# Kernel optimization log

Measured on AMD Instinct MI355X. Metric: run time of the kernel, lower is better.

Reference implementation:

```python
import jax, jax.numpy as jnp
import numpy as np

N, F, H, R, T, E, C = 50000, 128, 64, 3, 2, 500000, 2


def _seg_sum(v, idx, n):
    return jax.ops.segment_sum(v, idx, num_segments=n)


def _sage(x, src, dst, Wl, Wr, b, n):
    # PyG SAGEConv(mean): lin_l(mean_{j->i} x_j) + lin_r(x_i); lin_l carries bias.
    s = _seg_sum(x[src], dst, n)
    cnt = _seg_sum(jnp.ones((src.shape[0],), x.dtype), dst, n)
    agg = s / jnp.maximum(cnt, 1.0)[:, None]
    return agg @ Wl + x @ Wr + b


def _gcn(x, src, dst, w, W, b, n):
    # PyG GCNConv with edge_weight: self-loops (weight 1) + symmetric norm.
    deg = _seg_sum(w, dst, n) + 1.0
    dinv = deg ** -0.5
    norm = dinv[src] * w * dinv[dst]
    xW = x @ W
    return _seg_sum(norm[:, None] * xW[src], dst, n) + xW / deg[:, None] + b


def setup_inputs() -> dict:
    key = jax.random.key(0)
    ks = jax.random.split(key, 32)
    rn = lambda k, shp, s=0.1: jax.random.normal(k, shp, dtype=jnp.float32) * s
    return {
        "x": rn(ks[0], (N, F), 1.0),
        "edge_main": jax.random.randint(ks[1], (R, 2, E), 0, N, dtype=jnp.int32),
        "edge_tree": jax.random.randint(ks[2], (R, T, 2, E), 0, N, dtype=jnp.int32),
        "sage_Wl0": rn(ks[3], (R, F, H)), "sage_Wr0": rn(ks[4], (R, F, H)), "sage_b0": rn(ks[5], (R, H)),
        "sage_Wl1": rn(ks[6], (R, H, H)), "sage_Wr1": rn(ks[7], (R, H, H)), "sage_b1": rn(ks[8], (R, H)),
        "tree_Wl": rn(ks[9], (R, T, F, H)), "tree_Wr": rn(ks[10], (R, T, F, H)), "tree_b": rn(ks[11], (R, T, H)),
        "gate_W": rn(ks[12], (R, T, H)), "gate_b": rn(ks[13], (R, T)),
        "node_emb": rn(ks[14], (R, H), 1.0), "edge_emb": rn(ks[15], (R, H), 1.0),
        "fm_W": rn(ks[16], (R, 2 * H + F, F)), "fm_b": rn(ks[17], (R, F)),
        "ea_W1": rn(ks[18], (3 * H, F)), "ea_b1": rn(ks[19], (F,)),
        "ea_W2": rn(ks[20], (F, 1)), "ea_b2": rn(ks[21], (1,)),
        "gcn_W0": rn(ks[22], (R, F, H)), "gcn_b0": rn(ks[23], (R, H)),
        "gcn_W1": rn(ks[24], (R, H, H)), "gcn_b1": rn(ks[25], (R, H)),
        "lin_W": rn(ks[26], (R * H, C)), "lin_b": rn(ks[27], (C,)),
    }


def reference(x, edge_main, edge_tree, sage_Wl0, sage_Wr0, sage_b0, sage_Wl1, sage_Wr1, sage_b1,
              tree_Wl, tree_Wr, tree_b, gate_W, gate_b, node_emb, edge_emb, fm_W, fm_b,
              ea_W1, ea_b1, ea_W2, ea_b2, gcn_W0, gcn_b0, gcn_W1, gcn_b1, lin_W, lin_b):
    outs = []
    for r in range(R):
        src, dst = edge_main[r, 0], edge_main[r, 1]
        # Layer_AGG main SAGE stack (2 layers, relu between; dropout = eval no-op)
        y = jax.nn.relu(_sage(x, src, dst, sage_Wl0[r], sage_Wr0[r], sage_b0[r], N))
        y = _sage(y, src, dst, sage_Wl1[r], sage_Wr1[r], sage_b1[r], N)
        # tree branches + softmax gating
        trees = []
        for t in range(T):
            ts, td = edge_tree[r, t, 0], edge_tree[r, t, 1]
            trees.append(jax.nn.relu(_sage(x, ts, td, tree_Wl[r, t], tree_Wr[r, t], tree_b[r, t], N)))
        gates = jnp.stack([trees[t] @ gate_W[r, t] + gate_b[r, t] for t in range(T)], axis=-1)  # [N,T]
        alpha = jax.nn.softmax(gates, axis=-1)
        x_tree = sum(trees[t] * alpha[:, t:t + 1] for t in range(T))
        lo = y + 1.0 * x_tree  # self.weight = 1
        # edge mask via edge_attr_mlp on [lo[src], lo[dst], edge_type_emb]
        ef = jnp.concatenate([lo[src], lo[dst], jnp.broadcast_to(edge_emb[r], (E, H))], axis=-1)
        em = jax.nn.relu(ef @ ea_W1 + ea_b1) @ ea_W2 + ea_b2  # [E,1]
        # feature mask via feat_mask_r on [lo, x, node_type_emb]
        hetro = jnp.concatenate([lo, x, jnp.broadcast_to(node_emb[r], (N, H))], axis=-1)
        fm = hetro @ fm_W[r] + fm_b[r]
        mx = x * fm
        w = ((em - em.min()) / (em.max() - em.min()))[:, 0]  # min-max norm -> [E]
        # hetero GCN stack with edge weights
        z = jax.nn.relu(_gcn(mx, src, dst, w, gcn_W0[r], gcn_b0[r], N))
        z = _gcn(z, src, dst, w, gcn_W1[r], gcn_b1[r], N)
        outs.append(z)
    x_temp = jnp.concatenate(outs, axis=1)  # [N, R*H]
    logits = jnp.clip(x_temp @ lin_W + lin_b, -1e10, 1e10)
    return jax.nn.log_softmax(logits, axis=1), x_temp
```

## Files before the change

### kernel.cpp

```cpp
#include <hip/hip_runtime.h>
#include <cstdint>

#define N_NODES 50000
#define FEAT    128
#define HID     64
#define NREL    3
#define NTREE   2
#define NEDGE   500000
#define NCLS    2

#define BKT   391
#define CAP   1600
#define CHUNK 4096

typedef __attribute__((ext_vector_type(8))) short bfrag;
typedef __attribute__((ext_vector_type(4))) float ffrag;

__device__ __forceinline__ float wave_red(float v){
  #pragma unroll
  for(int off = 32; off > 0; off >>= 1) v += __shfl_xor(v, off, 64);
  return v;
}

__device__ __forceinline__ unsigned short f2b(float f){
// ... 102 lines not shown
    __syncthreads();
    if(tid < 128) sc[tid] += t;
    __syncthreads();
  }
  if(tid < 128){
    int excl = sc[tid] - h[tid];
    cur[tid] = excl;
    int node = b * 128 + tid;
    if(node < N_NODES) indptr9[(size_t)set * (N_NODES + 1) + node] = ebase + excl;
  }
  __syncthreads();
  for(int i = tid; i < cnt; i += 256){
    int p = pk[i];
    int r = atomicAdd(&cur[(p >> 16) & 127], 1);
    stage[r] = p & 0xFFFF;
  }
  __syncthreads();
  int* out = csr9 + (size_t)set * NEDGE + ebase;
  for(int i = tid; i < cnt; i += 256) out[i] = stage[i];
}

__global__ void k_tobf16(const float* __restrict__ in, unsigned short* __restrict__ o, int n4){
  int i = blockIdx.x * 256 + threadIdx.x;
  if(i < n4){
    float4 v = ((const float4*)in)[i];
    ushort4 u; u.x = f2b(v.x); u.y = f2b(v.y); u.z = f2b(v.z); u.w = f2b(v.w);
    ((ushort4*)o)[i] = u;
  }
}

struct PackJobs { const float* src[20]; int wst[20]; int K[20]; int dst[20]; int n; };

__global__ void k_wpack(PackJobs J, unsigned short* __restrict__ out){
  int j = blockIdx.x;
  if(j >= J.n) return;
  const float* s = J.src[j];
  int wst = J.wst[j], K = J.K[j];
  unsigned short* o = out + J.dst[j];
  for(int i = threadIdx.x; i < K * 64; i += 256){
    int k = i >> 6, c = i & 63;
    o[((((k >> 3) * 64) + c) << 3) + (k & 7)] = f2b(s[(size_t)k * wst + c]);
  }
}

struct MG {
  const unsigned short* Wt[4];
  const float* bias[4];
  const void* add[4];
  const float* mul[4];
  void* out[4];
  int ast, mst, ost;
};

template<int K1, int K2, int NGRP, int RELU, int HAS_ADD, int ADDB, int HAS_MUL, int OUT_BF16>
__global__ __launch_bounds__(256)
void k_mgemm(const unsigned short* __restrict__ X1, int xs1,
             const unsigned short* __restrict__ X2, int xs2, MG P){
  constexpr int K = K1 + K2;
  constexpr int KS = K / 32;
  int tid = threadIdx.x;
  int lane = tid & 63;
  int w = tid >> 6;
  int row0 = blockIdx.x * 64 + w * 16;
  int l15 = lane & 15, kg = lane >> 4;
  int arow = row0 + l15; if(arow > N_NODES - 1) arow = N_NODES - 1;
  bfrag a[KS];
  #pragma unroll
  for(int ks = 0; ks < KS; ks++){
    int kk = ks * 32 + kg * 8;
    const unsigned short* p = (kk < K1) ? (X1 + (size_t)arow * xs1 + kk)
                                        : (X2 + (size_t)arow * xs2 + (kk - K1));
    a[ks] = *(const bfrag*)p;
  }
  int orow0 = row0 + kg * 4;
  #pragma unroll
  for(int g = 0; g < NGRP; g++){
    const unsigned short* Wg = P.Wt[g];
    #pragma unroll
    for(int ct = 0; ct < 4; ct++){
      int col = ct * 16 + l15;
      ffrag acc = {0.f, 0.f, 0.f, 0.f};
      #pragma unroll
      for(int ks = 0; ks < KS; ks++){
        bfrag bf = *(const bfrag*)(Wg + (((size_t)(ks * 4 + kg) * 64 + col) << 3));
        acc = __builtin_amdgcn_mfma_f32_16x16x32_bf16(a[ks], bf, acc, 0, 0, 0);
      }
      float bv = P.bias[g] ? P.bias[g][col] : 0.f;
      #pragma unroll
      for(int i = 0; i < 4; i++){
        int r = orow0 + i;
        if(r >= N_NODES) break;
        float v = acc[i] + bv;
        if(HAS_ADD){
          if(ADDB) v += b2f(((const unsigned short*)P.add[g])[(size_t)r * P.ast + col]);
          else     v += ((const float*)P.add[g])[(size_t)r * P.ast + col];
        }
        if(RELU) v = fmaxf(v, 0.f);
        if(HAS_MUL) v *= P.mul[g][(size_t)r * P.mst + col];
        if(OUT_BF16) ((unsigned short*)P.out[g])[(size_t)r * P.ost + col] = f2b(v);
        else         ((float*)P.out[g])[(size_t)r * P.ost + col] = v;
      }
    }
  }
}

struct ABMX {
  const unsigned short* Wea[4];
  const unsigned short* Wfm[2];
  const float* cF;
  const float* xf32;
  unsigned short* ab;
  unsigned short* mx;
};

__global__ __launch_bounds__(256)
void k_abmx(const unsigned short* __restrict__ LOb, const unsigned short* __restrict__ xb, ABMX P){
  int tid = threadIdx.x, lane = tid & 63, w = tid >> 6;
  int row0 = blockIdx.x * 64 + w * 16;
  int l15 = lane & 15, kg = lane >> 4;
  int arow = row0 + l15; if(arow > N_NODES - 1) arow = N_NODES - 1;
  bfrag a[6];
  a[0] = *(const bfrag*)(LOb + (size_t)arow * 64 + kg * 8);
  a[1] = *(const bfrag*)(LOb + (size_t)arow * 64 + 32 + kg * 8);
  #pragma unroll
  for(int ks = 0; ks < 4; ks++)
    a[2 + ks] = *(const bfrag*)(xb + (size_t)arow * 128 + ks * 32 + kg * 8);
  int orow0 = row0 + kg * 4;
  #pragma unroll
  for(int g = 0; g < 4; g++){
    const unsigned short* Wg = P.Wea[g];
    #pragma unroll
    for(int ct = 0; ct < 4; ct++){
      int col = ct * 16 + l15;
      ffrag acc = {0.f, 0.f, 0.f, 0.f};
      bfrag b0 = *(const bfrag*)(Wg + (((size_t)(0 * 4 + kg) * 64 + col) << 3));
      bfrag b1 = *(const bfrag*)(Wg + (((size_t)(1 * 4 + kg) * 64 + col) << 3));
      acc = __builtin_amdgcn_mfma_f32_16x16x32_bf16(a[0], b0, acc, 0, 0, 0);
      acc = __builtin_amdgcn_mfma_f32_16x16x32_bf16(a[1], b1, acc, 0, 0, 0);
      #pragma unroll
      for(int i = 0; i < 4; i++){
        int r = orow0 + i;
        if(r >= N_NODES) break;
        P.ab[(size_t)r * 256 + g * 64 + col] = f2b(acc[i]);
      }
    }
  }
  #pragma unroll
  for(int g = 0; g < 2; g++){
    const unsigned short* Wg = P.Wfm[g];
    #pragma unroll
    for(int ct = 0; ct < 4; ct++){
      int col = ct * 16 + l15;
      ffrag acc = {0.f, 0.f, 0.f, 0.f};
      #pragma unroll
      for(int ks = 0; ks < 6; ks++){
        bfrag bf = *(const bfrag*)(Wg + (((size_t)(ks * 4 + kg) * 64 + col) << 3));
        acc = __builtin_amdgcn_mfma_f32_16x16x32_bf16(a[ks], bf, acc, 0, 0, 0);
      }
      float bv = P.cF[g * 64 + col];
      #pragma unroll
      for(int i = 0; i < 4; i++){
        int r = orow0 + i;
        if(r >= N_NODES) break;
        float v = (acc[i] + bv) * P.xf32[(size_t)r * 128 + g * 64 + col];
        P.mx[(size_t)r * 128 + g * 64 + col] = f2b(v);
      }
    }
  }
}

template<int OUTB>
__global__ void k_agg8(const unsigned short* __restrict__ TB, int tst,
                       const int* __restrict__ indptr, const int* __restrict__ csr,
                       void* __restrict__ out){
  int br = blockIdx.y;
  const unsigned short* T = TB + (size_t)br * tst;
  const int* ip = indptr + (size_t)br * (N_NODES + 1);
  const int* cs = csr + (size_t)br * NEDGE;
  int lane = threadIdx.x & 63, wid = threadIdx.x >> 6;
  int node = blockIdx.x * 4 + wid;
  if(node >= N_NODES) return;
  int q = lane >> 3, c = lane & 7;
  int beg = ip[node], end = ip[node + 1];
  int cnt = end - beg;
  float sc = 1.0f / (float)(cnt >= 1 ? cnt : 1);
  float a0=0.f,a1=0.f,a2=0.f,a3=0.f,a4=0.f,a5=0.f,a6=0.f,a7=0.f;
  int j = beg + q;
  for(; j + 8 < end; j += 16){
    int s0 = cs[j], s1 = cs[j + 8];
    uint4 u0 = *(const uint4*)(T + (size_t)s0 * 64 + c * 8);
    uint4 u1 = *(const uint4*)(T + (size_t)s1 * 64 + c * 8);
    a0 += b2f_lo(u0.x) + b2f_lo(u1.x); a1 += b2f_hi(u0.x) + b2f_hi(u1.x);
    a2 += b2f_lo(u0.y) + b2f_lo(u1.y); a3 += b2f_hi(u0.y) + b2f_hi(u1.y);
    a4 += b2f_lo(u0.z) + b2f_lo(u1.z); a5 += b2f_hi(u0.z) + b2f_hi(u1.z);
    a6 += b2f_lo(u0.w) + b2f_lo(u1.w); a7 += b2f_hi(u0.w) + b2f_hi(u1.w);
  }
  if(j < end){
    int s = cs[j];
    uint4 u = *(const uint4*)(T + (size_t)s * 64 + c * 8);
    a0 += b2f_lo(u.x); a1 += b2f_hi(u.x);
    a2 += b2f_lo(u.y); a3 += b2f_hi(u.y);
    a4 += b2f_lo(u.z); a5 += b2f_hi(u.z);
    a6 += b2f_lo(u.w); a7 += b2f_hi(u.w);
  }
  #pragma unroll
  for(int off = 8; off < 64; off <<= 1){
    a0 += __shfl_xor(a0, off, 64); a1 += __shfl_xor(a1, off, 64);
    a2 += __shfl_xor(a2, off, 64); a3 += __shfl_xor(a3, off, 64);
    a4 += __shfl_xor(a4, off, 64); a5 += __shfl_xor(a5, off, 64);
    a6 += __shfl_xor(a6, off, 64); a7 += __shfl_xor(a7, off, 64);
  }
  if(q == 0){
    if(OUTB){
      uint4 o;
      o.x = pk2(a0 * sc, a1 * sc); o.y = pk2(a2 * sc, a3 * sc);
      o.z = pk2(a4 * sc, a5 * sc); o.w = pk2(a6 * sc, a7 * sc);
      *(uint4*)((unsigned short*)out + (size_t)br * tst + (size_t)node * 64 + c * 8) = o;
    } else {
      float* o = (float*)out + (size_t)node * 64 + c * 8;
      *(float4*)o       = float4{a0 * sc, a1 * sc, a2 * sc, a3 * sc};
      *(float4*)(o + 4) = float4{a4 * sc, a5 * sc, a6 * sc, a7 * sc};
    }
  }
}

__global__ void k_gates_cvec(const unsigned short* __restrict__ t0b, const unsigned short* __restrict__ t1b,
                             const float* __restrict__ y, const float* __restrict__ gate_W,
                             const float* __restrict__ gate_b, unsigned short* __restrict__ lo,
                             const float* __restrict__ ee, const float* __restrict__ ne,
                             const float* __restrict__ eaW1, const float* __restrict__ eab1,
                             const float* __restrict__ fmW, const float* __restrict__ fmb,
                             float* __restrict__ cE, float* __restrict__ cF, int gn4){
  if(blockIdx.x >= gn4){
    int which = blockIdx.x - gn4;
    int j = threadIdx.x;
    if(j < 128){
      if(which == 0){
        float s = eab1[j];
        for(int k = 0; k < 64; k++) s += ee[k] * eaW1[(128 + k) * 128 + j];
        cE[j] = s;
      } else {
        float s = fmb[j];
        for(int k = 0; k < 64; k++) s += ne[k] * fmW[(192 + k) * 128 + j];
        cF[j] = s;
      }
    }
    return;
  }
  int lane = threadIdx.x & 63, wid = threadIdx.x >> 6;
  int node = blockIdx.x * 4 + wid;
  if(node >= N_NODES) return;
  size_t idx = (size_t)node * 64 + lane;
  float t0v = b2f(t0b[idx]), t1v = b2f(t1b[idx]), yv = y[idx];
  float g0 = wave_red(t0v * gate_W[lane]) + gate_b[0];
  float g1 = wave_red(t1v * gate_W[64 + lane]) + gate_b[1];
  float m = fmaxf(g0, g1);
  float e0 = expf(g0 - m), e1 = expf(g1 - m);
  float a0 = e0 / (e0 + e1);
  lo[idx] = f2b(yv + a0 * t0v + (1.f - a0) * t1v);
}

__global__ void k_em2(const unsigned short* __restrict__ AB,
                      const int* __restrict__ indptr, const int* __restrict__ csr_src,
                      const float* __restrict__ cvec, const float* __restrict__ W2,
                      const float* __restrict__ b2, float* __restrict__ em,
                      float* __restrict__ sumem, float* __restrict__ pmn, float* __restrict__ pmx){
  int lane = threadIdx.x & 63, wid = threadIdx.x >> 6;
  int node = blockIdx.x * 4 + wid;
  float mn = 3.4e38f, mx = -3.4e38f;
  if(node < N_NODES){
    int q = lane >> 4, c = lane & 15;
    uint4 bu = *(const uint4*)(AB + (size_t)node * 256 + 128 + c * 8);
    float4 cva = *(const float4*)&cvec[c * 8];
    float4 cvb = *(const float4*)&cvec[c * 8 + 4];
    float4 wva = *(const float4*)&W2[c * 8];
    float4 wvb = *(const float4*)&W2[c * 8 + 4];
    float cc0 = b2f_lo(bu.x) + cva.x, cc1 = b2f_hi(bu.x) + cva.y;
    float cc2 = b2f_lo(bu.y) + cva.z, cc3 = b2f_hi(bu.y) + cva.w;
    float cc4 = b2f_lo(bu.z) + cvb.x, cc5 = b2f_hi(bu.z) + cvb.y;
    float cc6 = b2f_lo(bu.w) + cvb.z, cc7 = b2f_hi(bu.w) + cvb.w;
    float b2v = b2[0];
    int beg = indptr[node], end = indptr[node + 1];
    float ssum = 0.f;
    int j = beg + q;
    for(; j + 4 < end; j += 8){
      int s0 = csr_src[j], s1 = csr_src[j + 4];
      uint4 u0 = *(const uint4*)(AB + (size_t)s0 * 256 + c * 8);
      uint4 u1 = *(const uint4*)(AB + (size_t)s1 * 256 + c * 8);
      float v0 = fmaxf(b2f_lo(u0.x) + cc0, 0.f) * wva.x + fmaxf(b2f_hi(u0.x) + cc1, 0.f) * wva.y
               + fmaxf(b2f_lo(u0.y) + cc2, 0.f) * wva.z + fmaxf(b2f_hi(u0.y) + cc3, 0.f) * wva.w
               + fmaxf(b2f_lo(u0.z) + cc4, 0.f) * wvb.x + fmaxf(b2f_hi(u0.z) + cc5, 0.f) * wvb.y
               + fmaxf(b2f_lo(u0.w) + cc6, 0.f) * wvb.z + fmaxf(b2f_hi(u0.w) + cc7, 0.f) * wvb.w;
      float v1 = fmaxf(b2f_lo(u1.x) + cc0, 0.f) * wva.x + fmaxf(b2f_hi(u1.x) + cc1, 0.f) * wva.y
               + fmaxf(b2f_lo(u1.y) + cc2, 0.f) * wva.z + fmaxf(b2f_hi(u1.y) + cc3, 0.f) * wva.w
               + fmaxf(b2f_lo(u1.z) + cc4, 0.f) * wvb.x + fmaxf(b2f_hi(u1.z) + cc5, 0.f) * wvb.y
               + fmaxf(b2f_lo(u1.w) + cc6, 0.f) * wvb.z + fmaxf(b2f_hi(u1.w) + cc7, 0.f) * wvb.w;
      #pragma unroll
      for(int off = 1; off < 16; off <<= 1){
        v0 += __shfl_xor(v0, off, 64);
        v1 += __shfl_xor(v1, off, 64);
      }
      float r0 = v0 + b2v, r1 = v1 + b2v;
      if(c == 0){ em[j] = r0; em[j + 4] = r1; }
      ssum += r0 + r1;
      mn = fminf(mn, fminf(r0, r1)); mx = fmaxf(mx, fmaxf(r0, r1));
    }
    if(j < end){
      int s = csr_src[j];
      uint4 u = *(const uint4*)(AB + (size_t)s * 256 + c * 8);
      float v = fmaxf(b2f_lo(u.x) + cc0, 0.f) * wva.x + fmaxf(b2f_hi(u.x) + cc1, 0.f) * wva.y
              + fmaxf(b2f_lo(u.y) + cc2, 0.f) * wva.z + fmaxf(b2f_hi(u.y) + cc3, 0.f) * wva.w
              + fmaxf(b2f_lo(u.z) + cc4, 0.f) * wvb.x + fmaxf(b2f_hi(u.z) + cc5, 0.f) * wvb.y
              + fmaxf(b2f_lo(u.w) + cc6, 0.f) * wvb.z + fmaxf(b2f_hi(u.w) + cc7, 0.f) * wvb.w;
      #pragma unroll
      for(int off = 1; off < 16; off <<= 1) v += __shfl_xor(v, off, 64);
      float r = v + b2v;
      if(c == 0) em[j] = r;
      ssum += r;
      mn = fminf(mn, r); mx = fmaxf(mx, r);
    }
    ssum += __shfl_xor(ssum, 16, 64); ssum += __shfl_xor(ssum, 32, 64);
    mn = fminf(mn, __shfl_xor(mn, 16, 64)); mn = fminf(mn, __shfl_xor(mn, 32, 64));
    mx = fmaxf(mx, __shfl_xor(mx, 16, 64)); mx = fmaxf(mx, __shfl_xor(mx, 32, 64));
    if(lane == 0) sumem[node] = ssum;
  }
  __shared__ float bmn[4], bmx[4];
  if(lane == 0){ bmn[wid] = mn; bmx[wid] = mx; }
  __syncthreads();
  if(threadIdx.x == 0){
    pmn[blockIdx.x] = fminf(fminf(bmn[0], bmn[1]), fminf(bmn[2], bmn[3]));
    pmx[blockIdx.x] = fmaxf(fmaxf(bmx[0], bmx[1]), fmaxf(bmx[2], bmx[3]));
  }
}

__global__ void k_minmax_final(const float* __restrict__ pmn, const float* __restrict__ pmx,
                               int nb, float* __restrict__ scal){
  __shared__ float smn[256], smx[256];
  int tid = threadIdx.x;
  float mn = 3.4e38f, mx = -3.4e38f;
  for(int i = tid; i < nb; i += 256){
    mn = fminf(mn, pmn[i]); mx = fmaxf(mx, pmx[i]);
  }
  smn[tid] = mn; smx[tid] = mx; __syncthreads();
  for(int s = 128; s > 0; s >>= 1){
    if(tid < s){ smn[tid] = fminf(smn[tid], smn[tid + s]); smx[tid] = fmaxf(smx[tid], smx[tid + s]); }
    __syncthreads();
  }
  if(tid == 0){
    scal[0] = smn[0];
    scal[1] = 1.0f / fmaxf(smx[0] - smn[0], 1e-30f);
  }
}

__global__ void k_dinv(const int* __restrict__ indptr, const float* __restrict__ sumem,
                       const float* __restrict__ scal, float* __restrict__ dinv){
  int i = blockIdx.x * 256 + threadIdx.x;
  if(i >= N_NODES) return;
  float mn = scal[0], inv = scal[1];
  float cnt = (float)(indptr[i + 1] - indptr[i]);
  dinv[i] = rsqrtf(1.f + (sumem[i] - cnt * mn) * inv);
}

template<int RELU, int OUTB>
__global__ void k_gcn(const unsigned short* __restrict__ xW, const int* __restrict__ indptr,
                      const int* __restrict__ csr_src, const float* __restrict__ em,
                      const float* __restrict__ scal, const float* __restrict__ dinv,
                      const float* __restrict__ bias, void* __restrict__ out, int ostride){
  int lane = threadIdx.x & 63, wid = threadIdx.x >> 6;
  int node = blockIdx.x * 4 + wid;
  if(node >= N_NODES) return;
  int q = lane >> 3, c = lane & 7;
  float mn = scal[0], inv = scal[1];
  float di = dinv[node];
  float a0=0.f,a1=0.f,a2=0.f,a3=0.f,a4=0.f,a5=0.f,a6=0.f,a7=0.f;
  int beg = indptr[node], end = indptr[node + 1];
  int j = beg + q;
  for(; j + 8 < end; j += 16){
    int s0 = csr_src[j], s1 = csr_src[j + 8];
    float w0 = (em[j] - mn) * inv * dinv[s0];
    float w1 = (em[j + 8] - mn) * inv * dinv[s1];
    uint4 u0 = *(const uint4*)(xW + (size_t)s0 * 64 + c * 8);
    uint4 u1 = *(const uint4*)(xW + (size_t)s1 * 64 + c * 8);
    a0 += w0 * b2f_lo(u0.x) + w1 * b2f_lo(u1.x); a1 += w0 * b2f_hi(u0.x) + w1 * b2f_hi(u1.x);
    a2 += w0 * b2f_lo(u0.y) + w1 * b2f_lo(u1.y); a3 += w0 * b2f_hi(u0.y) + w1 * b2f_hi(u1.y);
    a4 += w0 * b2f_lo(u0.z) + w1 * b2f_lo(u1.z); a5 += w0 * b2f_hi(u0.z) + w1 * b2f_hi(u1.z);
    a6 += w0 * b2f_lo(u0.w) + w1 * b2f_lo(u1.w); a7 += w0 * b2f_hi(u0.w) + w1 * b2f_hi(u1.w);
  }
  if(j < end){
    int s = csr_src[j];
    float wv = (em[j] - mn) * inv * dinv[s];
    uint4 u = *(const uint4*)(xW + (size_t)s * 64 + c * 8);
    a0 += wv * b2f_lo(u.x); a1 += wv * b2f_hi(u.x);
    a2 += wv * b2f_lo(u.y); a3 += wv * b2f_hi(u.y);
    a4 += wv * b2f_lo(u.z); a5 += wv * b2f_hi(u.z);
    a6 += wv * b2f_lo(u.w); a7 += wv * b2f_hi(u.w);
  }
  #pragma unroll
  for(int off = 8; off < 64; off <<= 1){
    a0 += __shfl_xor(a0, off, 64); a1 += __shfl_xor(a1, off, 64);
    a2 += __shfl_xor(a2, off, 64); a3 += __shfl_xor(a3, off, 64);
    a4 += __shfl_xor(a4, off, 64); a5 += __shfl_xor(a5, off, 64);
    a6 += __shfl_xor(a6, off, 64); a7 += __shfl_xor(a7, off, 64);
  }
  if(q == 0){
    uint4 su = *(const uint4*)(xW + (size_t)node * 64 + c * 8);
    float4 bva = *(const float4*)&bias[c * 8];
    float4 bvb = *(const float4*)&bias[c * 8 + 4];
    float dd = di * di;
    float r0 = a0 * di + b2f_lo(su.x) * dd + bva.x;
    float r1 = a1 * di + b2f_hi(su.x) * dd + bva.y;
    float r2 = a2 * di + b2f_lo(su.y) * dd + bva.z;
    float r3 = a3 * di + b2f_hi(su.y) * dd + bva.w;
    float r4 = a4 * di + b2f_lo(su.z) * dd + bvb.x;
// ... 33 lines not shown
  a1 = wave_red(a1);
  if(lane == 0){
    float l0 = fminf(fmaxf(a0 + lin_b[0], -1e10f), 1e10f);
    float l1 = fminf(fmaxf(a1 + lin_b[1], -1e10f), 1e10f);
    float m = fmaxf(l0, l1);
    float d = expf(l0 - m) + expf(l1 - m);
    float ls = m + logf(d);
    out[(size_t)node * 2 + 0] = l0 - ls;
    out[(size_t)node * 2 + 1] = l1 - ls;
  }
}

extern "C" void kernel_launch(void* const* d_in, const int* in_sizes, int n_in,
                              void* d_out, int out_size, void* d_ws, size_t ws_size,
                              hipStream_t stream){
  (void)in_sizes; (void)n_in; (void)out_size;
  const int N = N_NODES, E = NEDGE;

  const float* x        = (const float*)d_in[0];
  const int*  edge_main = (const int*)d_in[1];
  const int*  edge_tree = (const int*)d_in[2];
  const float* sage_Wl0 = (const float*)d_in[3];
  const float* sage_Wr0 = (const float*)d_in[4];
  const float* sage_b0  = (const float*)d_in[5];
  const float* sage_Wl1 = (const float*)d_in[6];
  const float* sage_Wr1 = (const float*)d_in[7];
  const float* sage_b1  = (const float*)d_in[8];
  const float* tree_Wl  = (const float*)d_in[9];
  const float* tree_Wr  = (const float*)d_in[10];
  const float* tree_b   = (const float*)d_in[11];
  const float* gate_W   = (const float*)d_in[12];
  const float* gate_b   = (const float*)d_in[13];
  const float* node_emb = (const float*)d_in[14];
  const float* edge_emb = (const float*)d_in[15];
  const float* fm_W     = (const float*)d_in[16];
  const float* fm_b     = (const float*)d_in[17];
  const float* ea_W1    = (const float*)d_in[18];
  const float* ea_b1    = (const float*)d_in[19];
  const float* ea_W2    = (const float*)d_in[20];
  const float* ea_b2    = (const float*)d_in[21];
  const float* gcn_W0   = (const float*)d_in[22];
  const float* gcn_b0   = (const float*)d_in[23];
  const float* gcn_W1   = (const float*)d_in[24];
  const float* gcn_b1   = (const float*)d_in[25];
  const float* lin_W    = (const float*)d_in[26];
  const float* lin_b    = (const float*)d_in[27];

  float* out_lsm   = (float*)d_out;
  float* out_xtemp = (float*)d_out + (size_t)N * NCLS;

  char* ws = (char*)d_ws;
  unsigned short* TB3  = (unsigned short*)(ws + 0);
  unsigned short* TBs  = (unsigned short*)(ws + 0);
  float*          Y    = (float*)(ws + 0);
  unsigned short* xW0b = (unsigned short*)(ws + 0);
  unsigned short* z0b  = (unsigned short*)(ws + 6400000);
  unsigned short* xW1b = (unsigned short*)(ws + 12800000);
  unsigned short* AG3  = (unsigned short*)(ws + 19200000);
  float*          AG   = (float*)(ws + 19200000);
  unsigned short* LOb  = (unsigned short*)(ws + 25600000);
  unsigned short* AB   = (unsigned short*)(ws + 0);
  unsigned short* y0b  = (unsigned short*)(ws + 38400000);
  unsigned short* T0b  = (unsigned short*)(ws + 44800000);
  unsigned short* T1b  = (unsigned short*)(ws + 51200000);
  unsigned short* MXb  = (unsigned short*)(ws + 38400000);
  unsigned short* xb   = (unsigned short*)(ws + 57600000);
  int*   bucketed = (int*)(ws + 0);
  unsigned short* Wpk = (unsigned short*)(ws + 70400000);
  int*   csr9     = (int*)(ws + 71000064);
  int*   indptr9  = (int*)(ws + 89000064);
  float* em       = (float*)(ws + 90800128);
  float* sumem    = (float*)(ws + 92800128);
  float* dinv     = (float*)(ws + 93000128);
  int*   cursor   = (int*)(ws + 93200128);
  int*   bktbase  = (int*)(ws + 93214208);
  float* cvecE    = (float*)(ws + 93228288);
  float* cvecF    = (float*)(ws + 93228800);
  float* scal     = (float*)(ws + 93229312);
  float* pmn      = (float*)(ws + 93229568);
  float* pmx      = (float*)(ws + 93279568);
  if(ws_size < 93330000) return;

  const int GN4 = (N + 3) / 4;
  const int GN  = (N + 255) / 256;
  const int GGM = (N + 63) / 64;
  const int NCH = (E + CHUNK - 1) / CHUNK;

  PackJobs PJ[2]; PJ[0].n = 0; PJ[1].n = 0;
  int npj = 0, dstElem = 0;
  const unsigned short* WlpA[NREL]; const unsigned short* WlpB[NREL]; const unsigned short* WlpC[NREL];
  const unsigned short* Wr0j[NREL]; const unsigned short* WrT0[NREL]; const unsigned short* WrT1[NREL];
  const unsigned short* Wl1j[NREL]; const unsigned short* Wr1j[NREL];
  const unsigned short* Fm0j[NREL]; const unsigned short* Fm1j[NREL];
  const unsigned short* G0j[NREL];  const unsigned short* G1j[NREL];
  const unsigned short *EaA0, *EaA1, *EaB0, *EaB1;
  auto addjob = [&](const float* src, int wst, int K) -> const unsigned short* {
    int slot = npj < 20 ? 0 : 1;
    int k = npj - slot * 20;
    PJ[slot].src[k] = src; PJ[slot].wst[k] = wst; PJ[slot].K[k] = K; PJ[slot].dst[k] = dstElem;
    PJ[slot].n = k + 1;
    const unsigned short* ret = Wpk + dstElem;
    dstElem += K * 64; npj++;
    return ret;
  };
  for(int r = 0; r < NREL; r++){
    WlpA[r] = addjob(sage_Wl0 + (size_t)r * 8192, 64, 128);
    WlpB[r] = addjob(tree_Wl + (size_t)(r * NTREE + 0) * 8192, 64, 128);
    WlpC[r] = addjob(tree_Wl + (size_t)(r * NTREE + 1) * 8192, 64, 128);
    Wr0j[r] = addjob(sage_Wr0 + (size_t)r * 8192, 64, 128);
    WrT0[r] = addjob(tree_Wr + (size_t)(r * NTREE + 0) * 8192, 64, 128);
    WrT1[r] = addjob(tree_Wr + (size_t)(r * NTREE + 1) * 8192, 64, 128);
    Wl1j[r] = addjob(sage_Wl1 + (size_t)r * 4096, 64, 64);
    Wr1j[r] = addjob(sage_Wr1 + (size_t)r * 4096, 64, 64);
    Fm0j[r] = addjob(fm_W + (size_t)r * 32768, 128, 192);
    Fm1j[r] = addjob(fm_W + (size_t)r * 32768 + 64, 128, 192);
    G0j[r]  = addjob(gcn_W0 + (size_t)r * 8192, 64, 128);
    G1j[r]  = addjob(gcn_W1 + (size_t)r * 4096, 64, 64);
  }
  EaA0 = addjob(ea_W1, 128, 64);
  EaA1 = addjob(ea_W1 + 64, 128, 64);
  EaB0 = addjob(ea_W1 + 64 * 128, 128, 64);
  EaB1 = addjob(ea_W1 + 64 * 128 + 64, 128, 64);

  EdgePtrs ep;
  for(int r = 0; r < NREL; r++){
    ep.s[r * 3 + 0] = edge_main + (size_t)r * 2 * E;
    ep.d[r * 3 + 0] = ep.s[r * 3 + 0] + E;
    for(int t = 0; t < NTREE; t++){
      ep.s[r * 3 + 1 + t] = edge_tree + ((size_t)(r * NTREE + t) * 2) * E;
      ep.d[r * 3 + 1 + t] = ep.s[r * 3 + 1 + t] + E;
    }
  }
  hipMemsetAsync(cursor, 0, 9 * BKT * 4, stream);
  k_passA<<<dim3(NCH, 9), 256, 0, stream>>>(ep, cursor, bucketed);
  k_scanB<<<9, 512, 0, stream>>>(cursor, bktbase, indptr9);
  k_passB<<<dim3(BKT, 9), 256, 0, stream>>>(bucketed, cursor, bktbase, indptr9, csr9);

  k_wpack<<<PJ[0].n, 256, 0, stream>>>(PJ[0], Wpk);
  k_wpack<<<PJ[1].n, 256, 0, stream>>>(PJ[1], Wpk);
  k_tobf16<<<(N * 128 / 4 + 255) / 256, 256, 0, stream>>>(x, xb, N * 128 / 4);

  for(int r = 0; r < NREL; r++){
    const int* ipM = indptr9 + (size_t)(r * 3) * (N + 1);
    const int* csM = csr9 + (size_t)(r * 3) * E;

    { MG p{}; p.ost = 64;
      p.Wt[0] = WlpA[r]; p.Wt[1] = WlpB[r]; p.Wt[2] = WlpC[r];
      p.out[0] = TB3; p.out[1] = TB3 + (size_t)N * 64; p.out[2] = TB3 + (size_t)2 * N * 64;
      k_mgemm<128, 0, 3, 0, 0, 0, 0, 1><<<GGM, 256, 0, stream>>>(xb, 128, nullptr, 0, p); }

    k_agg8<1><<<dim3(GN4, 3), 256, 0, stream>>>(TB3, N * 64, ipM, csM, AG3);
    { MG p{}; p.ast = 64; p.ost = 64;
      p.Wt[0] = Wr0j[r]; p.bias[0] = sage_b0 + r * 64; p.add[0] = AG3;                         p.out[0] = y0b;
      p.Wt[1] = WrT0[r]; p.bias[1] = tree_b + (size_t)(r * NTREE + 0) * 64; p.add[1] = AG3 + (size_t)N * 64;   p.out[1] = T0b;
      p.Wt[2] = WrT1[r]; p.bias[2] = tree_b + (size_t)(r * NTREE + 1) * 64; p.add[2] = AG3 + (size_t)2 * N * 64; p.out[2] = T1b;
      k_mgemm<128, 0, 3, 1, 1, 1, 0, 1><<<GGM, 256, 0, stream>>>(xb, 128, nullptr, 0, p); }

    { MG p{}; p.ost = 64; p.Wt[0] = Wl1j[r]; p.out[0] = TBs;
      k_mgemm<64, 0, 1, 0, 0, 0, 0, 1><<<GGM, 256, 0, stream>>>(y0b, 64, nullptr, 0, p); }
    k_agg8<0><<<dim3(GN4, 1), 256, 0, stream>>>(TBs, N * 64, ipM, csM, AG);
    { MG p{}; p.ast = 64; p.ost = 64;
      p.Wt[0] = Wr1j[r]; p.bias[0] = sage_b1 + r * 64; p.add[0] = AG; p.out[0] = Y;
      k_mgemm<64, 0, 1, 0, 1, 0, 0, 0><<<GGM, 256, 0, stream>>>(y0b, 64, nullptr, 0, p); }

    k_gates_cvec<<<GN4 + 2, 256, 0, stream>>>(T0b, T1b, Y, gate_W + (size_t)r * 128,
                                              gate_b + r * 2, LOb,
                                              edge_emb + r * 64, node_emb + r * 64,
                                              ea_W1, ea_b1, fm_W + (size_t)r * 32768,
                                              fm_b + r * 128, cvecE, cvecF, GN4);

    { ABMX p{};
      p.Wea[0] = EaA0; p.Wea[1] = EaA1; p.Wea[2] = EaB0; p.Wea[3] = EaB1;
      p.Wfm[0] = Fm0j[r]; p.Wfm[1] = Fm1j[r];
      p.cF = cvecF; p.xf32 = x; p.ab = AB; p.mx = MXb;
      k_abmx<<<GGM, 256, 0, stream>>>(LOb, xb, p); }

    k_em2<<<GN4, 256, 0, stream>>>(AB, ipM, csM, cvecE, ea_W2, ea_b2, em, sumem, pmn, pmx);

    k_minmax_final<<<1, 256, 0, stream>>>(pmn, pmx, GN4, scal);

    k_dinv<<<GN, 256, 0, stream>>>(ipM, sumem, scal, dinv);

    { MG p{}; p.ost = 64; p.Wt[0] = G0j[r]; p.out[0] = xW0b;
      k_mgemm<128, 0, 1, 0, 0, 0, 0, 1><<<GGM, 256, 0, stream>>>(MXb, 128, nullptr, 0, p); }
    k_gcn<1, 1><<<GN4, 256, 0, stream>>>(xW0b, ipM, csM, em, scal, dinv, gcn_b0 + r * 64, z0b, 64);
    { MG p{}; p.ost = 64; p.Wt[0] = G1j[r]; p.out[0] = xW1b;
      k_mgemm<64, 0, 1, 0, 0, 0, 0, 1><<<GGM, 256, 0, stream>>>(z0b, 64, nullptr, 0, p); }
    k_gcn<0, 0><<<GN4, 256, 0, stream>>>(xW1b, ipM, csM, em, scal, dinv, gcn_b1 + r * 64,
                                         out_xtemp + r * 64, 192);
  }

  k_logits<<<GN4, 256, 0, stream>>>(out_xtemp, lin_W, lin_b, out_lsm);
}
```

Baseline: 892.5 us.

## Fuse SAGE/tree GEMMs, gating and GCN xW0 into chained kernels per relation

Merges the post-aggregation SAGE/tree GEMM with the next layer's Wl1 projection through an LDS tile, fuses the Wr1 GEMM with tree gating and the lo computation, and chains the feature-mask product into the GCN layer-0 GEMM via shared memory. The min/max finalisation is folded into the dinv kernel, with each block redoing the small reduction. The aggregation kernel now uses 16 lanes of 4 columns per edge instead of 8 lanes of 8. The goal is fewer launches and fewer global round trips for intermediates such as Y, MX and the separate xW0 pass. The cost is extra LDS use and redundant reductions, and the workspace buffer aliasing is reshuffled.

```diff
diff --git a/kernel.cpp b/kernel.cpp
--- a/kernel.cpp
+++ b/kernel.cpp
@@ -178,12 +178,10 @@
   int ast, mst, ost;
 };
 
-template<int K1, int K2, int NGRP, int RELU, int HAS_ADD, int ADDB, int HAS_MUL, int OUT_BF16>
+template<int K1, int NGRP, int OUT_BF16>
 __global__ __launch_bounds__(256)
-void k_mgemm(const unsigned short* __restrict__ X1, int xs1,
-             const unsigned short* __restrict__ X2, int xs2, MG P){
-  constexpr int K = K1 + K2;
-  constexpr int KS = K / 32;
+void k_mgemm(const unsigned short* __restrict__ X1, int xs1, MG P){
+  constexpr int KS = K1 / 32;
   int tid = threadIdx.x;
   int lane = tid & 63;
   int w = tid >> 6;
@@ -192,12 +190,8 @@
   int arow = row0 + l15; if(arow > N_NODES - 1) arow = N_NODES - 1;
   bfrag a[KS];
   #pragma unroll
-  for(int ks = 0; ks < KS; ks++){
-    int kk = ks * 32 + kg * 8;
-    const unsigned short* p = (kk < K1) ? (X1 + (size_t)arow * xs1 + kk)
-                                        : (X2 + (size_t)arow * xs2 + (kk - K1));
-    a[ks] = *(const bfrag*)p;
-  }
+  for(int ks = 0; ks < KS; ks++)
+    a[ks] = *(const bfrag*)(X1 + (size_t)arow * xs1 + ks * 32 + kg * 8);
   int orow0 = row0 + kg * 4;
   #pragma unroll
   for(int g = 0; g < NGRP; g++){
@@ -211,18 +205,11 @@
         bfrag bf = *(const bfrag*)(Wg + (((size_t)(ks * 4 + kg) * 64 + col) << 3));
         acc = __builtin_amdgcn_mfma_f32_16x16x32_bf16(a[ks], bf, acc, 0, 0, 0);
       }
-      float bv = P.bias[g] ? P.bias[g][col] : 0.f;
       #pragma unroll
       for(int i = 0; i < 4; i++){
         int r = orow0 + i;
         if(r >= N_NODES) break;
-        float v = acc[i] + bv;
-        if(HAS_ADD){
-          if(ADDB) v += b2f(((const unsigned short*)P.add[g])[(size_t)r * P.ast + col]);
-          else     v += ((const float*)P.add[g])[(size_t)r * P.ast + col];
-        }
-        if(RELU) v = fmaxf(v, 0.f);
-        if(HAS_MUL) v *= P.mul[g][(size_t)r * P.mst + col];
+        float v = acc[i];
         if(OUT_BF16) ((unsigned short*)P.out[g])[(size_t)r * P.ost + col] = f2b(v);
         else         ((float*)P.out[g])[(size_t)r * P.ost + col] = v;
       }
@@ -230,17 +217,182 @@
   }
 }
 
-struct ABMX {
+struct S23 {
+  const unsigned short* Wr[3];
+  const float* bias[3];
+  const unsigned short* ag3;
+  const unsigned short* Wl1;
+  unsigned short *y0, *t0, *t1, *tbs;
+};
+
+__global__ __launch_bounds__(256)
+void k_s23(const unsigned short* __restrict__ xb, S23 P){
+  __shared__ unsigned short ytile[64][72];
+  int tid = threadIdx.x, lane = tid & 63, w = tid >> 6;
+  int row0 = blockIdx.x * 64 + w * 16;
+  int l15 = lane & 15, kg = lane >> 4;
+  int arow = row0 + l15; if(arow > N_NODES - 1) arow = N_NODES - 1;
+  bfrag a[4];
+  #pragma unroll
+  for(int ks = 0; ks < 4; ks++)
+    a[ks] = *(const bfrag*)(xb + (size_t)arow * 128 + ks * 32 + kg * 8);
+  int orow0 = row0 + kg * 4;
+  #pragma unroll
+  for(int g = 0; g < 3; g++){
+    const unsigned short* Wg = P.Wr[g];
+    unsigned short* og = (g == 0) ? P.y0 : (g == 1) ? P.t0 : P.t1;
+    #pragma unroll
+    for(int ct = 0; ct < 4; ct++){
+      int col = ct * 16 + l15;
+      ffrag acc = {0.f, 0.f, 0.f, 0.f};
+      #pragma unroll
+      for(int ks = 0; ks < 4; ks++){
+        bfrag bf = *(const bfrag*)(Wg + (((size_t)(ks * 4 + kg) * 64 + col) << 3));
+        acc = __builtin_amdgcn_mfma_f32_16x16x32_bf16(a[ks], bf, acc, 0, 0, 0);
+      }
+      float bv = P.bias[g][col];
+      #pragma unroll
+      for(int i = 0; i < 4; i++){
+        int r = orow0 + i;
+        int rr = (r < N_NODES) ? r : N_NODES - 1;
+        float v = acc[i] + bv + b2f(P.ag3[(size_t)g * N_NODES * 64 + (size_t)rr * 64 + col]);
+        v = fmaxf(v, 0.f);
+        unsigned short hh = f2b(v);
+        if(g == 0) ytile[w * 16 + kg * 4 + i][col] = hh;
+        if(r < N_NODES) og[(size_t)r * 64 + col] = hh;
+      }
+    }
+  }
+  __syncthreads();
+  bfrag a2[2];
+  a2[0] = *(const bfrag*)&ytile[w * 16 + l15][kg * 8];
+  a2[1] = *(const bfrag*)&ytile[w * 16 + l15][32 + kg * 8];
+  #pragma unroll
+  for(int ct = 0; ct < 4; ct++){
+    int col = ct * 16 + l15;
+    ffrag acc = {0.f, 0.f, 0.f, 0.f};
+    bfrag b0 = *(const bfrag*)(P.Wl1 + (((size_t)(0 * 4 + kg) * 64 + col) << 3));
+    bfrag b1 = *(const bfrag*)(P.Wl1 + (((size_t)(1 * 4 + kg) * 64 + col) << 3));
+    acc = __builtin_amdgcn_mfma_f32_16x16x32_bf16(a2[0], b0, acc, 0, 0, 0);
+    acc = __builtin_amdgcn_mfma_f32_16x16x32_bf16(a2[1], b1, acc, 0, 0, 0);
+    #pragma unroll
+    for(int i = 0; i < 4; i++){
+      int r = orow0 + i;
+      if(r >= N_NODES) break;
+      P.tbs[(size_t)r * 64 + col] = f2b(acc[i]);
+    }
+  }
+}
+
+struct YG {
+  const unsigned short* Wr1;
+  const float* b1;
+  const float* AG;
+  const unsigned short *t0b, *t1b;
+  const float *gate_W, *gate_b;
+  unsigned short* lo;
+  const float *ee, *ne, *eaW1, *eab1, *fmW, *fmb;
+  float *cE, *cF;
+  int ggm;
+};
+
+__global__ __launch_bounds__(256)
+void k_ygates(const unsigned short* __restrict__ y0b, YG P){
+  if(blockIdx.x >= P.ggm){
+    int which = blockIdx.x - P.ggm;
+    int j = threadIdx.x;
+    if(j < 128){
+      if(which == 0){
+        float s = P.eab1[j];
+        for(int k = 0; k < 64; k++) s += P.ee[k] * P.eaW1[(128 + k) * 128 + j];
+        P.cE[j] = s;
+      } else {
+        float s = P.fmb[j];
+        for(int k = 0; k < 64; k++) s += P.ne[k] * P.fmW[(192 + k) * 128 + j];
+        P.cF[j] = s;
+      }
+    }
+    return;
+  }
+  int tid = threadIdx.x, lane = tid & 63, w = tid >> 6;
+  int row0 = blockIdx.x * 64 + w * 16;
+  int l15 = lane & 15, kg = lane >> 4;
+  int arow = row0 + l15; if(arow > N_NODES - 1) arow = N_NODES - 1;
+  bfrag a0f = *(const bfrag*)(y0b + (size_t)arow * 64 + kg * 8);
+  bfrag a1f = *(const bfrag*)(y0b + (size_t)arow * 64 + 32 + kg * 8);
+  int orow0 = row0 + kg * 4;
+  float vv[4][4], t0v[4][4], t1v[4][4];
+  float gw0[4], gw1[4];
+  #pragma unroll
+  for(int ct = 0; ct < 4; ct++){
+    int col = ct * 16 + l15;
+    gw0[ct] = P.gate_W[col];
+    gw1[ct] = P.gate_W[64 + col];
+  }
+  #pragma unroll
+  for(int ct = 0; ct < 4; ct++){
+    int col = ct * 16 + l15;
+    ffrag acc = {0.f, 0.f, 0.f, 0.f};
+    bfrag b0 = *(const bfrag*)(P.Wr1 + (((size_t)(0 * 4 + kg) * 64 + col) << 3));
+    bfrag b1 = *(const bfrag*)(P.Wr1 + (((size_t)(1 * 4 + kg) * 64 + col) << 3));
+    acc = __builtin_amdgcn_mfma_f32_16x16x32_bf16(a0f, b0, acc, 0, 0, 0);
+    acc = __builtin_amdgcn_mfma_f32_16x16x32_bf16(a1f, b1, acc, 0, 0, 0);
+    float bv = P.b1[col];
+    #pragma unroll
+    for(int i = 0; i < 4; i++){
+      int r = orow0 + i;
+      int rr = (r < N_NODES) ? r : N_NODES - 1;
+      vv[i][ct] = acc[i] + bv + P.AG[(size_t)rr * 64 + col];
+      t0v[i][ct] = b2f(P.t0b[(size_t)rr * 64 + col]);
+      t1v[i][ct] = b2f(P.t1b[(size_t)rr * 64 + col]);
+    }
+  }
+  float pg0[4] = {0.f, 0.f, 0.f, 0.f}, pg1[4] = {0.f, 0.f, 0.f, 0.f};
+  #pragma unroll
+  for(int i = 0; i < 4; i++)
+    #pragma unroll
+    for(int ct = 0; ct < 4; ct++){
+      pg0[i] += t0v[i][ct] * gw0[ct];
+      pg1[i] += t1v[i][ct] * gw1[ct];
+    }
+  #pragma unroll
+  for(int off = 1; off < 16; off <<= 1){
+    #pragma unroll
+    for(int i = 0; i < 4; i++){
+      pg0[i] += __shfl_xor(pg0[i], off, 64);
+      pg1[i] += __shfl_xor(pg1[i], off, 64);
+    }
+  }
+  float gb0 = P.gate_b[0], gb1 = P.gate_b[1];
+  #pragma unroll
+  for(int i = 0; i < 4; i++){
+    int r = orow0 + i;
+    if(r >= N_NODES) break;
+    float g0 = pg0[i] + gb0, g1 = pg1[i] + gb1;
+    float m = fmaxf(g0, g1);
+    float e0 = expf(g0 - m), e1 = expf(g1 - m);
+    float av = e0 / (e0 + e1);
+    #pragma unroll
+    for(int ct = 0; ct < 4; ct++){
+      int col = ct * 16 + l15;
+      P.lo[(size_t)r * 64 + col] = f2b(vv[i][ct] + av * t0v[i][ct] + (1.f - av) * t1v[i][ct]);
+    }
+  }
+}
+
+struct ABMX2 {
   const unsigned short* Wea[4];
   const unsigned short* Wfm[2];
+  const unsigned short* G0;
   const float* cF;
   const float* xf32;
   unsigned short* ab;
-  unsigned short* mx;
+  unsigned short* xw0;
 };
 
 __global__ __launch_bounds__(256)
-void k_abmx(const unsigned short* __restrict__ LOb, const unsigned short* __restrict__ xb, ABMX P){
+void k_abmx2(const unsigned short* __restrict__ LOb, const unsigned short* __restrict__ xb, ABMX2 P){
+  __shared__ unsigned short mxtile[64][136];
   int tid = threadIdx.x, lane = tid & 63, w = tid >> 6;
   int row0 = blockIdx.x * 64 + w * 16;
   int l15 = lane & 15, kg = lane >> 4;
@@ -287,16 +439,37 @@
       #pragma unroll
       for(int i = 0; i < 4; i++){
         int r = orow0 + i;
-        if(r >= N_NODES) break;
-        float v = (acc[i] + bv) * P.xf32[(size_t)r * 128 + g * 64 + col];
-        P.mx[(size_t)r * 128 + g * 64 + col] = f2b(v);
-      }
+        int rr = (r < N_NODES) ? r : N_NODES - 1;
+        float v = (acc[i] + bv) * P.xf32[(size_t)rr * 128 + g * 64 + col];
+        mxtile[w * 16 + kg * 4 + i][g * 64 + col] = f2b(v);
+      }
+    }
+  }
+  __syncthreads();
+  bfrag a3[4];
+  #pragma unroll
+  for(int ks = 0; ks < 4; ks++)
+    a3[ks] = *(const bfrag*)&mxtile[w * 16 + l15][ks * 32 + kg * 8];
+  #pragma unroll
+  for(int ct = 0; ct < 4; ct++){
+    int col = ct * 16 + l15;
+    ffrag acc = {0.f, 0.f, 0.f, 0.f};
+    #pragma unroll
+    for(int ks = 0; ks < 4; ks++){
+      bfrag bf = *(const bfrag*)(P.G0 + (((size_t)(ks * 4 + kg) * 64 + col) << 3));
+      acc = __builtin_amdgcn_mfma_f32_16x16x32_bf16(a3[ks], bf, acc, 0, 0, 0);
+    }
+    #pragma unroll
+    for(int i = 0; i < 4; i++){
+      int r = orow0 + i;
+      if(r >= N_NODES) break;
+      P.xw0[(size_t)r * 64 + col] = f2b(acc[i]);
     }
   }
 }
 
 template<int OUTB>
-__global__ void k_agg8(const unsigned short* __restrict__ TB, int tst,
+__global__ void k_aggq(const unsigned short* __restrict__ TB, int tst,
                        const int* __restrict__ indptr, const int* __restrict__ csr,
                        void* __restrict__ out){
   int br = blockIdx.y;
@@ -306,84 +479,37 @@
   int lane = threadIdx.x & 63, wid = threadIdx.x >> 6;
   int node = blockIdx.x * 4 + wid;
   if(node >= N_NODES) return;
-  int q = lane >> 3, c = lane & 7;
+  int q = lane >> 4, c = lane & 15;
   int beg = ip[node], end = ip[node + 1];
   int cnt = end - beg;
   float sc = 1.0f / (float)(cnt >= 1 ? cnt : 1);
-  float a0=0.f,a1=0.f,a2=0.f,a3=0.f,a4=0.f,a5=0.f,a6=0.f,a7=0.f;
+  float a0 = 0.f, a1 = 0.f, a2 = 0.f, a3 = 0.f;
   int j = beg + q;
-  for(; j + 8 < end; j += 16){
-    int s0 = cs[j], s1 = cs[j + 8];
-    uint4 u0 = *(const uint4*)(T + (size_t)s0 * 64 + c * 8);
-    uint4 u1 = *(const uint4*)(T + (size_t)s1 * 64 + c * 8);
+  for(; j + 4 < end; j += 8){
+    int s0 = cs[j], s1 = cs[j + 4];
+    uint2 u0 = *(const uint2*)(T + (size_t)s0 * 64 + c * 4);
+    uint2 u1 = *(const uint2*)(T + (size_t)s1 * 64 + c * 4);
     a0 += b2f_lo(u0.x) + b2f_lo(u1.x); a1 += b2f_hi(u0.x) + b2f_hi(u1.x);
     a2 += b2f_lo(u0.y) + b2f_lo(u1.y); a3 += b2f_hi(u0.y) + b2f_hi(u1.y);
-    a4 += b2f_lo(u0.z) + b2f_lo(u1.z); a5 += b2f_hi(u0.z) + b2f_hi(u1.z);
-    a6 += b2f_lo(u0.w) + b2f_lo(u1.w); a7 += b2f_hi(u0.w) + b2f_hi(u1.w);
   }
   if(j < end){
     int s = cs[j];
-    uint4 u = *(const uint4*)(T + (size_t)s * 64 + c * 8);
+    uint2 u = *(const uint2*)(T + (size_t)s * 64 + c * 4);
     a0 += b2f_lo(u.x); a1 += b2f_hi(u.x);
     a2 += b2f_lo(u.y); a3 += b2f_hi(u.y);
-    a4 += b2f_lo(u.z); a5 += b2f_hi(u.z);
-    a6 += b2f_lo(u.w); a7 += b2f_hi(u.w);
-  }
-  #pragma unroll
-  for(int off = 8; off < 64; off <<= 1){
-    a0 += __shfl_xor(a0, off, 64); a1 += __shfl_xor(a1, off, 64);
-    a2 += __shfl_xor(a2, off, 64); a3 += __shfl_xor(a3, off, 64);
-    a4 += __shfl_xor(a4, off, 64); a5 += __shfl_xor(a5, off, 64);
-    a6 += __shfl_xor(a6, off, 64); a7 += __shfl_xor(a7, off, 64);
-  }
+  }
+  a0 += __shfl_xor(a0, 16, 64); a1 += __shfl_xor(a1, 16, 64);
+  a2 += __shfl_xor(a2, 16, 64); a3 += __shfl_xor(a3, 16, 64);
+  a0 += __shfl_xor(a0, 32, 64); a1 += __shfl_xor(a1, 32, 64);
+  a2 += __shfl_xor(a2, 32, 64); a3 += __shfl_xor(a3, 32, 64);
   if(q == 0){
     if(OUTB){
-      uint4 o;
-      o.x = pk2(a0 * sc, a1 * sc); o.y = pk2(a2 * sc, a3 * sc);
-      o.z = pk2(a4 * sc, a5 * sc); o.w = pk2(a6 * sc, a7 * sc);
-      *(uint4*)((unsigned short*)out + (size_t)br * tst + (size_t)node * 64 + c * 8) = o;
+      ushort4 o; o.x = f2b(a0 * sc); o.y = f2b(a1 * sc); o.z = f2b(a2 * sc); o.w = f2b(a3 * sc);
+      *(ushort4*)((unsigned short*)out + (size_t)br * tst + (size_t)node * 64 + c * 4) = o;
     } else {
-      float* o = (float*)out + (size_t)node * 64 + c * 8;
-      *(float4*)o       = float4{a0 * sc, a1 * sc, a2 * sc, a3 * sc};
-      *(float4*)(o + 4) = float4{a4 * sc, a5 * sc, a6 * sc, a7 * sc};
-    }
-  }
-}
-
-__global__ void k_gates_cvec(const unsigned short* __restrict__ t0b, const unsigned short* __restrict__ t1b,
-                             const float* __restrict__ y, const float* __restrict__ gate_W,
-                             const float* __restrict__ gate_b, unsigned short* __restrict__ lo,
-                             const float* __restrict__ ee, const float* __restrict__ ne,
-                             const float* __restrict__ eaW1, const float* __restrict__ eab1,
-                             const float* __restrict__ fmW, const float* __restrict__ fmb,
-                             float* __restrict__ cE, float* __restrict__ cF, int gn4){
-  if(blockIdx.x >= gn4){
-    int which = blockIdx.x - gn4;
-    int j = threadIdx.x;
-    if(j < 128){
-      if(which == 0){
-        float s = eab1[j];
-        for(int k = 0; k < 64; k++) s += ee[k] * eaW1[(128 + k) * 128 + j];
-        cE[j] = s;
-      } else {
-        float s = fmb[j];
-        for(int k = 0; k < 64; k++) s += ne[k] * fmW[(192 + k) * 128 + j];
-        cF[j] = s;
-      }
-    }
-    return;
-  }
-  int lane = threadIdx.x & 63, wid = threadIdx.x >> 6;
-  int node = blockIdx.x * 4 + wid;
-  if(node >= N_NODES) return;
-  size_t idx = (size_t)node * 64 + lane;
-  float t0v = b2f(t0b[idx]), t1v = b2f(t1b[idx]), yv = y[idx];
-  float g0 = wave_red(t0v * gate_W[lane]) + gate_b[0];
-  float g1 = wave_red(t1v * gate_W[64 + lane]) + gate_b[1];
-  float m = fmaxf(g0, g1);
-  float e0 = expf(g0 - m), e1 = expf(g1 - m);
-  float a0 = e0 / (e0 + e1);
-  lo[idx] = f2b(yv + a0 * t0v + (1.f - a0) * t1v);
+      *(float4*)((float*)out + (size_t)node * 64 + c * 4) = float4{a0 * sc, a1 * sc, a2 * sc, a3 * sc};
+    }
+  }
 }
 
 __global__ void k_em2(const unsigned short* __restrict__ AB,
@@ -459,8 +585,9 @@
   }
 }
 
-__global__ void k_minmax_final(const float* __restrict__ pmn, const float* __restrict__ pmx,
-                               int nb, float* __restrict__ scal){
+__global__ void k_dinv2(const int* __restrict__ indptr, const float* __restrict__ sumem,
+                        const float* __restrict__ pmn, const float* __restrict__ pmx, int nb,
+                        float* __restrict__ scal, float* __restrict__ dinv){
   __shared__ float smn[256], smx[256];
   int tid = threadIdx.x;
   float mn = 3.4e38f, mx = -3.4e38f;
@@ -472,19 +599,13 @@
     if(tid < s){ smn[tid] = fminf(smn[tid], smn[tid + s]); smx[tid] = fmaxf(smx[tid], smx[tid + s]); }
     __syncthreads();
   }
-  if(tid == 0){
-    scal[0] = smn[0];
-    scal[1] = 1.0f / fmaxf(smx[0] - smn[0], 1e-30f);
-  }
-}
-
-__global__ void k_dinv(const int* __restrict__ indptr, const float* __restrict__ sumem,
-                       const float* __restrict__ scal, float* __restrict__ dinv){
-  int i = blockIdx.x * 256 + threadIdx.x;
+  float mn0 = smn[0];
+  float inv = 1.0f / fmaxf(smx[0] - mn0, 1e-30f);
+  if(blockIdx.x == 0 && tid == 0){ scal[0] = mn0; scal[1] = inv; }
+  int i = blockIdx.x * 256 + tid;
   if(i >= N_NODES) return;
-  float mn = scal[0], inv = scal[1];
   float cnt = (float)(indptr[i + 1] - indptr[i]);
-  dinv[i] = rsqrtf(1.f + (sumem[i] - cnt * mn) * inv);
+  dinv[i] = rsqrtf(1.f + (sumem[i] - cnt * mn0) * inv);
 }
 
 template<int RELU, int OUTB>
@@ -624,18 +745,16 @@
   char* ws = (char*)d_ws;
   unsigned short* TB3  = (unsigned short*)(ws + 0);
   unsigned short* TBs  = (unsigned short*)(ws + 0);
-  float*          Y    = (float*)(ws + 0);
-  unsigned short* xW0b = (unsigned short*)(ws + 0);
-  unsigned short* z0b  = (unsigned short*)(ws + 6400000);
-  unsigned short* xW1b = (unsigned short*)(ws + 12800000);
+  unsigned short* AB   = (unsigned short*)(ws + 0);
   unsigned short* AG3  = (unsigned short*)(ws + 19200000);
   float*          AG   = (float*)(ws + 19200000);
-  unsigned short* LOb  = (unsigned short*)(ws + 25600000);
-  unsigned short* AB   = (unsigned short*)(ws + 0);
+  unsigned short* LOb  = (unsigned short*)(ws + 32000000);
   unsigned short* y0b  = (unsigned short*)(ws + 38400000);
+  unsigned short* xW0b = (unsigned short*)(ws + 38400000);
   unsigned short* T0b  = (unsigned short*)(ws + 44800000);
+  unsigned short* z0b  = (unsigned short*)(ws + 44800000);
   unsigned short* T1b  = (unsigned short*)(ws + 51200000);
-  unsigned short* MXb  = (unsigned short*)(ws + 38400000);
+  unsigned short* xW1b = (unsigned short*)(ws + 51200000);
   unsigned short* xb   = (unsigned short*)(ws + 57600000);
   int*   bucketed = (int*)(ws + 0);
   unsigned short* Wpk = (unsigned short*)(ws + 70400000);
@@ -719,45 +838,45 @@
     { MG p{}; p.ost = 64;
       p.Wt[0] = WlpA[r]; p.Wt[1] = WlpB[r]; p.Wt[2] = WlpC[r];
       p.out[0] = TB3; p.out[1] = TB3 + (size_t)N * 64; p.out[2] = TB3 + (size_t)2 * N * 64;
-      k_mgemm<128, 0, 3, 0, 0, 0, 0, 1><<<GGM, 256, 0, stream>>>(xb, 128, nullptr, 0, p); }
-
-    k_agg8<1><<<dim3(GN4, 3), 256, 0, stream>>>(TB3, N * 64, ipM, csM, AG3);
-    { MG p{}; p.ast = 64; p.ost = 64;
-      p.Wt[0] = Wr0j[r]; p.bias[0] = sage_b0 + r * 64; p.add[0] = AG3;                         p.out[0] = y0b;
-      p.Wt[1] = WrT0[r]; p.bias[1] = tree_b + (size_t)(r * NTREE + 0) * 64; p.add[1] = AG3 + (size_t)N * 64;   p.out[1] = T0b;
-      p.Wt[2] = WrT1[r]; p.bias[2] = tree_b + (size_t)(r * NTREE + 1) * 64; p.add[2] = AG3 + (size_t)2 * N * 64; p.out[2] = T1b;
-      k_mgemm<128, 0, 3, 1, 1, 1, 0, 1><<<GGM, 256, 0, stream>>>(xb, 128, nullptr, 0, p); }
-
-    { MG p{}; p.ost = 64; p.Wt[0] = Wl1j[r]; p.out[0] = TBs;
-      k_mgemm<64, 0, 1, 0, 0, 0, 0, 1><<<GGM, 256, 0, stream>>>(y0b, 64, nullptr, 0, p); }
-    k_agg8<0><<<dim3(GN4, 1), 256, 0, stream>>>(TBs, N * 64, ipM, csM, AG);
-    { MG p{}; p.ast = 64; p.ost = 64;
-      p.Wt[0] = Wr1j[r]; p.bias[0] = sage_b1 + r * 64; p.add[0] = AG; p.out[0] = Y;
-      k_mgemm<64, 0, 1, 0, 1, 0, 0, 0><<<GGM, 256, 0, stream>>>(y0b, 64, nullptr, 0, p); }
-
-    k_gates_cvec<<<GN4 + 2, 256, 0, stream>>>(T0b, T1b, Y, gate_W + (size_t)r * 128,
-                                              gate_b + r * 2, LOb,
-                                              edge_emb + r * 64, node_emb + r * 64,
-                                              ea_W1, ea_b1, fm_W + (size_t)r * 32768,
-                                              fm_b + r * 128, cvecE, cvecF, GN4);
-
-    { ABMX p{};
+      k_mgemm<128, 3, 1><<<GGM, 256, 0, stream>>>(xb, 128, p); }
+
+    k_aggq<1><<<dim3(GN4, 3), 256, 0, stream>>>(TB3, N * 64, ipM, csM, AG3);
+
+    { S23 p{};
+      p.Wr[0] = Wr0j[r]; p.bias[0] = sage_b0 + r * 64;
+      p.Wr[1] = WrT0[r]; p.bias[1] = tree_b + (size_t)(r * NTREE + 0) * 64;
+      p.Wr[2] = WrT1[r]; p.bias[2] = tree_b + (size_t)(r * NTREE + 1) * 64;
+      p.ag3 = AG3; p.Wl1 = Wl1j[r];
+      p.y0 = y0b; p.t0 = T0b; p.t1 = T1b; p.tbs = TBs;
+      k_s23<<<GGM, 256, 0, stream>>>(xb, p); }
+
+    k_aggq<0><<<dim3(GN4, 1), 256, 0, stream>>>(TBs, N * 64, ipM, csM, AG);
+
+    { YG p{};
+      p.Wr1 = Wr1j[r]; p.b1 = sage_b1 + r * 64; p.AG = AG;
+      p.t0b = T0b; p.t1b = T1b;
+      p.gate_W = gate_W + (size_t)r * 128; p.gate_b = gate_b + r * 2;
+      p.lo = LOb;
+      p.ee = edge_emb + r * 64; p.ne = node_emb + r * 64;
+      p.eaW1 = ea_W1; p.eab1 = ea_b1;
+      p.fmW = fm_W + (size_t)r * 32768; p.fmb = fm_b + r * 128;
+      p.cE = cvecE; p.cF = cvecF; p.ggm = GGM;
+      k_ygates<<<GGM + 2, 256, 0, stream>>>(y0b, p); }
+
+    { ABMX2 p{};
       p.Wea[0] = EaA0; p.Wea[1] = EaA1; p.Wea[2] = EaB0; p.Wea[3] = EaB1;
       p.Wfm[0] = Fm0j[r]; p.Wfm[1] = Fm1j[r];
-      p.cF = cvecF; p.xf32 = x; p.ab = AB; p.mx = MXb;
-      k_abmx<<<GGM, 256, 0, stream>>>(LOb, xb, p); }
+      p.G0 = G0j[r]; p.cF = cvecF; p.xf32 = x;
+      p.ab = AB; p.xw0 = xW0b;
+      k_abmx2<<<GGM, 256, 0, stream>>>(LOb, xb, p); }
 
     k_em2<<<GN4, 256, 0, stream>>>(AB, ipM, csM, cvecE, ea_W2, ea_b2, em, sumem, pmn, pmx);
 
-    k_minmax_final<<<1, 256, 0, stream>>>(pmn, pmx, GN4, scal);
-
-    k_dinv<<<GN, 256, 0, stream>>>(ipM, sumem, scal, dinv);
-
-    { MG p{}; p.ost = 64; p.Wt[0] = G0j[r]; p.out[0] = xW0b;
-      k_mgemm<128, 0, 1, 0, 0, 0, 0, 1><<<GGM, 256, 0, stream>>>(MXb, 128, nullptr, 0, p); }
+    k_dinv2<<<GN, 256, 0, stream>>>(ipM, sumem, pmn, pmx, GN4, scal, dinv);
+
     k_gcn<1, 1><<<GN4, 256, 0, stream>>>(xW0b, ipM, csM, em, scal, dinv, gcn_b0 + r * 64, z0b, 64);
     { MG p{}; p.ost = 64; p.Wt[0] = G1j[r]; p.out[0] = xW1b;
-      k_mgemm<64, 0, 1, 0, 0, 0, 0, 1><<<GGM, 256, 0, stream>>>(z0b, 64, nullptr, 0, p); }
+      k_mgemm<64, 1, 1><<<GGM, 256, 0, stream>>>(z0b, 64, p); }
     k_gcn<0, 0><<<GN4, 256, 0, stream>>>(xW1b, ipM, csM, em, scal, dinv, gcn_b1 + r * 64,
                                          out_xtemp + r * 64, 192);
   }
```

Measured after the change: 799.5 us (median of 2 runs). 1.12x faster.
